# Kernel optimization log

Hardware: AMD Instinct MI355X
Metric: run time of the kernel (lower is better)

The kernel has to match this reference:

```python
import jax, jax.numpy as jnp
import numpy as np

B, L, D = 4, 8192, 512


def _normalize(v):
    # F.normalize: v / max(||v||, 1e-12)
    n = jnp.linalg.norm(v, axis=-1, keepdims=True)
    return v / jnp.maximum(n, 1e-12)


def setup_inputs() -> dict:
    key = jax.random.key(0)
    k1, k2, k3, k4 = jax.random.split(key, 4)
    return {
        "hidden_states": jax.random.normal(k1, (B, L, D), jnp.float32),
        "residual": jax.random.normal(k2, (B, L, D), jnp.float32),
        "q_weight": jax.random.normal(k3, (D, D), jnp.float32) * 0.02,
        "k_weight": jax.random.normal(k4, (D, D), jnp.float32) * 0.02,
        "det_state": jnp.zeros((B, D), jnp.float32),
    }


def reference(hidden_states, residual, q_weight, k_weight, det_state):
    Bs, Ls, Ds = hidden_states.shape
    # ---- CosineSimRouter.prob_boundary ----
    q = _normalize(hidden_states[:, :-1] @ q_weight.T)   # (B, L-1, D)
    k = _normalize(hidden_states[:, 1:] @ k_weight.T)    # (B, L-1, D)
    cos_sim = jnp.einsum('bld,bld->bl', q, k)            # (B, L-1)
    prob = jnp.concatenate(
        [jnp.ones((Bs, 1), jnp.float32), jnp.clip((1.0 - cos_sim) / 2.0, 0.0, 1.0)],
        axis=1)                                           # (B, L); prob[:,0]=1 (state=None path)
    token_mask = prob > 0.5                               # (B, L)

    # ---- Tokenizer: compact boundary positions (pad M -> L, static shape) ----
    counts = token_mask.sum(axis=1)                       # (B,)
    order = jnp.argsort(~token_mask, axis=1)              # stable: True-mask indices first, in order
    valid = jnp.arange(Ls)[None, :] < counts[:, None]     # (B, L)
    chunked = jnp.take_along_axis(hidden_states, order[..., None], axis=1)
    chunked = chunked * valid[..., None]                  # (B, L, D)
    chunk_probs = jnp.take_along_axis(prob, order, axis=1) * valid  # (B, L)

    # ---- DeTokenizer: EMA associative scan over compacted chunks ----
    decay = jnp.clip(1.0 - chunk_probs, 0.0, 1.0)
    # pad positions have chunk_probs=0 -> decay=1 -> state carried unchanged
    a = jnp.broadcast_to(decay[..., None], (Bs, Ls, Ds))
    b = (1.0 - decay)[..., None] * chunked
    b = b.at[:, 0].add(a[:, 0] * det_state)

    def comb(x, y):  # x earlier, y later: (a2*a1, a2*b1 + b2)
        ax, bx = x
        ay, by = y
        return ax * ay, ay * bx + by

    _, ema_out = jax.lax.associative_scan(comb, (a, b), axis=1)
    ema_out = ema_out * valid[..., None]                  # zero padded chunk slots

    # broadcast back to full sequence via cumulative chunk indexing
    chunk_idx = jnp.cumsum(token_mask.astype(jnp.int32), axis=1) - 1  # (B, L)
    ci = jnp.clip(chunk_idx, 0, Ls - 1)
    long_states = jnp.take_along_axis(ema_out, ci[..., None], axis=1)
    long_states = long_states * (chunk_idx >= 0)[..., None]

    # STE coefficient: forward == 1 (grad flows through max(1-p, p) in bwd)
    coef_raw = jnp.maximum(1.0 - prob, prob)
    coef = coef_raw + jax.lax.stop_gradient(1.0 - coef_raw)
    long_states = long_states * coef[..., None]

    output = residual + long_states                       # (B, L, D)
    return output
```

## Files before the change

### kernel.cpp

```cpp
#include <hip/hip_runtime.h>
#include <hip/hip_bf16.h>
#include <math.h>

#define B_  4
#define L_  8192
#define D_  512

#define BM   128
#define NCT  4
#define NRT  (L_ / BM)
#define KW   64
#define NSTAGE (D_ / KW)

#define CHUNK 64
#define NCHUNK (L_ / CHUNK)

#define MAXFIX 16380
#define FIX_TAU 1.0e-3f
#define FTILE 4

typedef short bf16x8 __attribute__((ext_vector_type(8)));
typedef float f32x4 __attribute__((ext_vector_type(4)));
typedef unsigned short u16;
typedef unsigned int u32;

__device__ __forceinline__ u32 pk2(float lo, float hi) {
    __hip_bfloat162 v = __float22bfloat162_rn(float2{lo, hi});
    union { __hip_bfloat162 b; u32 u; } cv; cv.b = v;
    return cv.u;
}

__global__ __launch_bounds__(256) void prep_w(
    const float* __restrict__ wq, const float* __restrict__ wk,
    u16* __restrict__ qh, u16* __restrict__ kh,
    float* __restrict__ wqt, float* __restrict__ wkt,
    int* __restrict__ fix_cnt)
{
    __shared__ float tile[64][65];
    const int bi = blockIdx.x;
    const int bj = blockIdx.y;
    const int t = threadIdx.x;
    if (bi == 0 && bj == 0 && t == 0) *fix_cnt = 0;
    const int c0 = bi * 64, k0 = bj * 64;
    const float* src = wq; float* dst = wqt; u16* dsth = qh;
#pragma unroll
    for (int m = 0; m < 2; ++m) {
        __syncthreads();
#pragma unroll
        for (int it = 0; it < 4; ++it) {
            int r = it * 16 + (t >> 4);
            int cc = (t & 15) * 4;
            float4 v = *(const float4*)(src + (size_t)(c0 + r) * D_ + k0 + cc);
            tile[r][cc] = v.x; tile[r][cc + 1] = v.y;
            tile[r][cc + 2] = v.z; tile[r][cc + 3] = v.w;
            uint2 hv; hv.x = pk2(v.x, v.y); hv.y = pk2(v.z, v.w);
            *(uint2*)(dsth + (size_t)(c0 + r) * D_ + k0 + cc) = hv;
        }
        __syncthreads();
#pragma unroll
        for (int it = 0; it < 4; ++it) {
            int cl = t & 63;
            int kq = it * 4 + (t >> 6);
            float4 v;
            v.x = tile[cl][kq * 4 + 0]; v.y = tile[cl][kq * 4 + 1];
            v.z = tile[cl][kq * 4 + 2]; v.w = tile[cl][kq * 4 + 3];
            size_t o = ((size_t)((k0 >> 2) + kq) * 512 + (c0 + cl)) * 4;
            *(float4*)(dst + o) = v;
        }
        src = wk; dst = wkt; dsth = kh;
    }
}

__global__ __launch_bounds__(256, 2) void qk_mfma(
    const float* __restrict__ h,
    const u16* __restrict__ wqh, const u16* __restrict__ wkh,
    float* __restrict__ part)
{
    const int bid = blockIdx.x;
    const int swz = (bid & 7) * 128 + (bid >> 3);
    const int ct = swz & 3, rt = (swz >> 2) & 63, b = swz >> 8;
    const int t = threadIdx.x, wid = t >> 6, lane = t & 63;
    const int l15 = lane & 15, l4 = lane >> 4;

    __shared__ __align__(16) u16 ah[129 * 64];
    __shared__ float red[4][BM][3];

    const int r0 = rt * BM;
    const float* hb = h + (size_t)b * L_ * D_;

    const int tr = t >> 4, q = t & 15;
    const float* gp = hb + (size_t)(r0 + tr) * D_ + q * 4;
    const int re = (r0 + BM > L_ - 1) ? (L_ - 1) : (r0 + BM);
    const float* gpe = hb + (size_t)re * D_ + q * 4;
    const int dbase = tr * 64 + (((q >> 1) ^ (tr & 7)) * 8) + ((q & 1) * 4);
    const int dE = 128 * 64 + ((t >> 1) * 8) + ((t & 1) * 4);

    const int colb = ct * 128 + wid * 32;
    const u16* bq0 = wqh + (size_t)(colb + l15) * D_ + l4 * 8;
    const u16* bq1 = bq0 + (size_t)16 * D_;
    const u16* bk0 = wkh + (size_t)(colb + l15) * D_ + l4 * 8;
    const u16* bk1 = bk0 + (size_t)16 * D_;

    int aoff[8];
#pragma unroll
    for (int rf = 0; rf < 8; ++rf) {
        int R = rf * 16 + l15;
        aoff[rf] = R * 64 + ((l4 ^ (R & 7)) * 8);
    }
    const int aoffE = 128 * 64 + l4 * 8;

    f32x4 accq[8][2], acck[8][2], ackl[2];
    const f32x4 zero = {0.f, 0.f, 0.f, 0.f};
#pragma unroll
    for (int rf = 0; rf < 8; ++rf) {
        accq[rf][0] = zero; accq[rf][1] = zero;
        acck[rf][0] = zero; acck[rf][1] = zero;
    }
    ackl[0] = zero; ackl[1] = zero;

    float4 A0, A1, A2, A3, A4, A5, A6, A7;
    float4 AE = {0.f, 0.f, 0.f, 0.f};

#define LOADA(S) do { const int _o = (S) * KW;                      \
    A0 = *(const float4*)(gp + _o);                                 \
    A1 = *(const float4*)(gp + _o + 8192);                          \
    A2 = *(const float4*)(gp + _o + 16384);                         \
    A3 = *(const float4*)(gp + _o + 24576);                         \
    A4 = *(const float4*)(gp + _o + 32768);                         \
    A5 = *(const float4*)(gp + _o + 40960);                         \
    A6 = *(const float4*)(gp + _o + 49152);                         \
    A7 = *(const float4*)(gp + _o + 57344);                         \
    if (t < 16) AE = *(const float4*)(gpe + _o); } while (0)

#define ST1(J, AV) { uint2 _h; _h.x = pk2(AV.x, AV.y); _h.y = pk2(AV.z, AV.w); \
    *(uint2*)(&ah[dbase + (J) * 1024]) = _h; }

    LOADA(0);
    for (int s = 0; s < NSTAGE; ++s) {
        __syncthreads();
        ST1(0, A0) ST1(1, A1) ST1(2, A2) ST1(3, A3)
        ST1(4, A4) ST1(5, A5) ST1(6, A6) ST1(7, A7)
        if (t < 16) { uint2 _h; _h.x = pk2(AE.x, AE.y); _h.y = pk2(AE.z, AE.w);
                      *(uint2*)(&ah[dE]) = _h; }

        const int so = s * KW;
        bf16x8 q00 = *(const bf16x8*)(bq0 + so);
        bf16x8 q01 = *(const bf16x8*)(bq0 + so + 32);
        bf16x8 q10 = *(const bf16x8*)(bq1 + so);
        bf16x8 q11 = *(const bf16x8*)(bq1 + so + 32);
        bf16x8 k00 = *(const bf16x8*)(bk0 + so);
        bf16x8 k01 = *(const bf16x8*)(bk0 + so + 32);
        bf16x8 k10 = *(const bf16x8*)(bk1 + so);
        bf16x8 k11 = *(const bf16x8*)(bk1 + so + 32);

        if (s + 1 < NSTAGE) LOADA(s + 1);
        __syncthreads();

#pragma unroll
        for (int kk = 0; kk < 2; ++kk) {
            bf16x8 fq0 = kk ? q01 : q00;
            bf16x8 fq1 = kk ? q11 : q10;
            bf16x8 fk0 = kk ? k01 : k00;
            bf16x8 fk1 = kk ? k11 : k10;
#pragma unroll
            for (int rf = 0; rf < 8; ++rf) {
                bf16x8 a = *(const bf16x8*)(&ah[aoff[rf] ^ (kk * 32)]);
                accq[rf][0] = __builtin_amdgcn_mfma_f32_16x16x32_bf16(a, fq0, accq[rf][0], 0, 0, 0);
                accq[rf][1] = __builtin_amdgcn_mfma_f32_16x16x32_bf16(a, fq1, accq[rf][1], 0, 0, 0);
                acck[rf][0] = __builtin_amdgcn_mfma_f32_16x16x32_bf16(a, fk0, acck[rf][0], 0, 0, 0);
                acck[rf][1] = __builtin_amdgcn_mfma_f32_16x16x32_bf16(a, fk1, acck[rf][1], 0, 0, 0);
            }
            bf16x8 al = *(const bf16x8*)(&ah[aoffE ^ (kk * 32)]);
            ackl[0] = __builtin_amdgcn_mfma_f32_16x16x32_bf16(al, fk0, ackl[0], 0, 0, 0);
            ackl[1] = __builtin_amdgcn_mfma_f32_16x16x32_bf16(al, fk1, ackl[1], 0, 0, 0);
        }
    }
#undef LOADA
#undef ST1

#pragma unroll
    for (int rf = 0; rf < 8; ++rf) {
#pragma unroll
        for (int reg = 0; reg < 4; ++reg) {
            float pq = 0.f, pk = 0.f, pd = 0.f;
#pragma unroll
            for (int cf = 0; cf < 2; ++cf) {
                float qv = accq[rf][cf][reg];
                float kv = acck[rf][cf][reg];
                pq += qv * qv;
                pk += kv * kv;
                float ksh;
                if (reg < 3) {
                    ksh = acck[rf][cf][reg + 1];
                } else {
                    float up = __shfl(acck[rf][cf][0], (lane + 16) & 63);
                    float nx0 = (rf < 7) ? acck[rf + 1][cf][0] : ackl[cf][0];
                    float nx = __shfl(nx0, l15);
                    ksh = (l4 == 3) ? nx : up;
                }
                pd += qv * ksh;
            }
#pragma unroll
            for (int off = 1; off < 16; off <<= 1) {
                pq += __shfl_xor(pq, off);
                pk += __shfl_xor(pk, off);
                pd += __shfl_xor(pd, off);
            }
            if (l15 == 0) {
                int row = rf * 16 + l4 * 4 + reg;
                red[wid][row][0] = pq;
                red[wid][row][1] = pk;
                red[wid][row][2] = pd;
            }
        }
    }
    __syncthreads();
    if (t < BM) {
        float pq = red[0][t][0] + red[1][t][0] + red[2][t][0] + red[3][t][0];
        float pk = red[0][t][1] + red[1][t][1] + red[2][t][1] + red[3][t][1];
        float pd = red[0][t][2] + red[1][t][2] + red[2][t][2] + red[3][t][2];
        size_t o = (((size_t)ct * B_ + b) * L_ + (r0 + t)) * 3;
        part[o + 0] = pq; part[o + 1] = pk; part[o + 2] = pd;
    }
}

__global__ __launch_bounds__(256) void cos_reduce(
    const float* __restrict__ part, float* __restrict__ p,
    int* __restrict__ fix_cnt, int* __restrict__ fix_list)
{
    int idx = blockIdx.x * 256 + threadIdx.x;
    if (idx >= B_ * L_) return;
    int b = idx / L_;
    int tp = idx % L_;
    if (tp == 0) { p[idx] = 1.0f; return; }
    int l = tp - 1;
    float nq = 0.f, nk = 0.f, dt = 0.f;
#pragma unroll
    for (int ct = 0; ct < NCT; ++ct) {
        size_t o = (((size_t)ct * B_ + b) * L_ + l) * 3;
        nq += part[o + 0];
        dt += part[o + 2];
        nk += part[o + 4];
    }
    float qn = sqrtf(nq); if (qn < 1e-12f) qn = 1e-12f;
    float kn = sqrtf(nk); if (kn < 1e-12f) kn = 1e-12f;
    float cs = dt / (qn * kn);
    float pr = 0.5f * (1.0f - cs);
    pr = fminf(fmaxf(pr, 0.0f), 1.0f);
    p[idx] = pr;
    if (fabsf(cs) < FIX_TAU) {
        int slot = atomicAdd(fix_cnt, 1);
        if (slot < MAXFIX) fix_list[slot] = idx;
    }
}

__global__ __launch_bounds__(256) void fixup_main(
    const float* __restrict__ h,
    const float* __restrict__ wqt, const float* __restrict__ wkt,
    const int* __restrict__ fix_cnt, const int* __restrict__ fix_list,
    float* __restrict__ p)
{
    __shared__ float hq[FTILE][D_];
    __shared__ float hk[FTILE][D_];
    __shared__ float red[FTILE][3][4];
    const int t = threadIdx.x, wid = t >> 6, lane = t & 63;
    int n = *fix_cnt; if (n > MAXFIX) n = MAXFIX;
    const int ntiles = (n + FTILE - 1) / FTILE;

    for (int tile = blockIdx.x; tile < ntiles; tile += gridDim.x) {
        __syncthreads();
#pragma unroll
        for (int r = 0; r < FTILE; ++r) {
            int s = tile * FTILE + r;
            int idx = fix_list[s < n ? s : 0];
            int bb = idx >> 13;
            int tp = idx & (L_ - 1);
            const float* hr = h + ((size_t)bb * L_ + (tp - 1)) * D_;
            ((float2*)hq[r])[t] = ((const float2*)hr)[t];
            ((float2*)hk[r])[t] = ((const float2*)(hr + D_))[t];
        }
        __syncthreads();

        float qa0[FTILE], qa1[FTILE], ka0[FTILE], ka1[FTILE];
#pragma unroll
        for (int r = 0; r < FTILE; ++r) { qa0[r] = qa1[r] = ka0[r] = ka1[r] = 0.f; }

        float4 wc0 = *(const float4*)(wqt + ((size_t)0 * 512 + t) * 4);
        float4 wc1 = *(const float4*)(wqt + ((size_t)0 * 512 + t + 256) * 4);
        float4 xc0 = *(const float4*)(wkt + ((size_t)0 * 512 + t) * 4);
        float4 xc1 = *(const float4*)(wkt + ((size_t)0 * 512 + t + 256) * 4);
#pragma unroll 4
        for (int kq = 0; kq < D_ / 4; ++kq) {
            const int kn = (kq + 1) & (D_ / 4 - 1);
            float4 wn0 = *(const float4*)(wqt + ((size_t)kn * 512 + t) * 4);
            float4 wn1 = *(const float4*)(wqt + ((size_t)kn * 512 + t + 256) * 4);
            float4 xn0 = *(const float4*)(wkt + ((size_t)kn * 512 + t) * 4);
            float4 xn1 = *(const float4*)(wkt + ((size_t)kn * 512 + t + 256) * 4);
#pragma unroll
            for (int r = 0; r < FTILE; ++r) {
                float4 hv = *(const float4*)(&hq[r][kq * 4]);
                float4 kv = *(const float4*)(&hk[r][kq * 4]);
                qa0[r] += hv.x * wc0.x + hv.y * wc0.y + hv.z * wc0.z + hv.w * wc0.w;
                qa1[r] += hv.x * wc1.x + hv.y * wc1.y + hv.z * wc1.z + hv.w * wc1.w;
                ka0[r] += kv.x * xc0.x + kv.y * xc0.y + kv.z * xc0.z + kv.w * xc0.w;
                ka1[r] += kv.x * xc1.x + kv.y * xc1.y + kv.z * xc1.z + kv.w * xc1.w;
            }
            wc0 = wn0; wc1 = wn1; xc0 = xn0; xc1 = xn1;
        }

#pragma unroll
        for (int r = 0; r < FTILE; ++r) {
            float pq = qa0[r] * qa0[r] + qa1[r] * qa1[r];
            float pk = ka0[r] * ka0[r] + ka1[r] * ka1[r];
            float pd = qa0[r] * ka0[r] + qa1[r] * ka1[r];
#pragma unroll
            for (int off = 1; off < 64; off <<= 1) {
                pq += __shfl_xor(pq, off);
                pk += __shfl_xor(pk, off);
                pd += __shfl_xor(pd, off);
            }
            if (lane == 0) { red[r][0][wid] = pq; red[r][1][wid] = pk; red[r][2][wid] = pd; }
        }
        __syncthreads();
        if (t < FTILE) {
            int s = tile * FTILE + t;
            if (s < n) {
                float nq = red[t][0][0] + red[t][0][1] + red[t][0][2] + red[t][0][3];
                float nk = red[t][1][0] + red[t][1][1] + red[t][1][2] + red[t][1][3];
                float dt = red[t][2][0] + red[t][2][1] + red[t][2][2] + red[t][2][3];
                float qn = sqrtf(nq); if (qn < 1e-12f) qn = 1e-12f;
                float kn = sqrtf(nk); if (kn < 1e-12f) kn = 1e-12f;
                float cs = dt / (qn * kn);
                float pr = 0.5f * (1.0f - cs);
                pr = fminf(fmaxf(pr, 0.0f), 1.0f);
                p[fix_list[s]] = pr;
            }
        }
    }
}

__global__ __launch_bounds__(256) void scan_a(
    const float* __restrict__ h, const float* __restrict__ p,
    float* __restrict__ Bc, float* __restrict__ Ac)
{
    const int t = threadIdx.x;
    const int c = blockIdx.x, b = blockIdx.y;
    const int l0 = c * CHUNK;
    const float* pb = p + (size_t)b * L_ + l0;
    const float2* hb = (const float2*)(h + ((size_t)b * L_ + l0) * D_) + t;

    float2 st = {0.f, 0.f};
    float ap = 1.f;
#pragma unroll 4
    for (int i = 0; i < CHUNK; ++i) {
        float pr = pb[i];
        float2 hv = hb[(size_t)i * 256];
        bool sel = pr > 0.5f;
        float a = sel ? 1.f - pr : 1.f;
        float g = sel ? pr : 0.f;
        st.x = a * st.x + g * hv.x;
        st.y = a * st.y + g * hv.y;
        ap *= a;
    }
    ((float2*)Bc)[((size_t)b * NCHUNK + c) * 256 + t] = st;
    if (t == 0) Ac[b * NCHUNK + c] = ap;
}

__global__ __launch_bounds__(256) void scan_b(
    const float* __restrict__ Ac, const float* __restrict__ Bc,
    const float* __restrict__ det, float* __restrict__ carry)
{
    const int t = threadIdx.x;
    const int b = blockIdx.x;
    const float* acb = Ac + b * NCHUNK;
    const float2* bcb = (const float2*)Bc + (size_t)b * NCHUNK * 256 + t;
    float2* cb = (float2*)carry + (size_t)b * NCHUNK * 256 + t;
    float2 st = ((const float2*)det)[(size_t)b * 256 + t];

    float a0 = acb[0], a1 = acb[1], a2 = acb[2], a3 = acb[3];
    float2 b0 = bcb[0], b1 = bcb[256], b2 = bcb[512], b3 = bcb[768];
    for (int g = 0; g < NCHUNK / 4; ++g) {
        const int nc = (g + 1 < NCHUNK / 4) ? (g + 1) * 4 : g * 4;
        float an0 = acb[nc], an1 = acb[nc + 1], an2 = acb[nc + 2], an3 = acb[nc + 3];
        float2 bn0 = bcb[(size_t)nc * 256],        bn1 = bcb[(size_t)(nc + 1) * 256];
        float2 bn2 = bcb[(size_t)(nc + 2) * 256],  bn3 = bcb[(size_t)(nc + 3) * 256];
        const size_t c0 = (size_t)g * 4 * 256;
        cb[c0]       = st; st.x = a0 * st.x + b0.x; st.y = a0 * st.y + b0.y;
        cb[c0 + 256] = st; st.x = a1 * st.x + b1.x; st.y = a1 * st.y + b1.y;
        cb[c0 + 512] = st; st.x = a2 * st.x + b2.x; st.y = a2 * st.y + b2.y;
        cb[c0 + 768] = st; st.x = a3 * st.x + b3.x; st.y = a3 * st.y + b3.y;
        a0 = an0; a1 = an1; a2 = an2; a3 = an3;
        b0 = bn0; b1 = bn1; b2 = bn2; b3 = bn3;
    }
}

__global__ __launch_bounds__(256) void scan_c(
    const float* __restrict__ h, const float* __restrict__ p,
    const float* __restrict__ res, const float* __restrict__ carry,
    float* __restrict__ out)
{
    const int t = threadIdx.x;
    const int c = blockIdx.x, b = blockIdx.y;
    const int l0 = c * CHUNK;
    const float* pb = p + (size_t)b * L_ + l0;
    const size_t base = ((size_t)b * L_ + l0) * 256 + t;
    const float2* hb = (const float2*)h + base;
    const float2* rb = (const float2*)res + base;
    float2* ob = (float2*)out + base;

    float2 st = ((const float2*)carry)[((size_t)b * NCHUNK + c) * 256 + t];
#pragma unroll 4
    for (int i = 0; i < CHUNK; ++i) {
        float pr = pb[i];
        float2 hv = hb[(size_t)i * 256];
        float2 rv = rb[(size_t)i * 256];
        bool sel = pr > 0.5f;
        float a = sel ? 1.f - pr : 1.f;
        float g = sel ? pr : 0.f;
        st.x = a * st.x + g * hv.x;
        st.y = a * st.y + g * hv.y;
        float2 ov; ov.x = rv.x + st.x; ov.y = rv.y + st.y;
        ob[(size_t)i * 256] = ov;
    }
}

extern "C" void kernel_launch(void* const* d_in, const int* in_sizes, int n_in,
                              void* d_out, int out_size, void* d_ws, size_t ws_size,
                              hipStream_t stream)
{
    const float* h   = (const float*)d_in[0];
    const float* res = (const float*)d_in[1];
    const float* wq  = (const float*)d_in[2];
    const float* wk  = (const float*)d_in[3];
    const float* det = (const float*)d_in[4];
    float* out = (float*)d_out;

    float* ws = (float*)d_ws;
    float* part  = ws;
    float* p     = part + (size_t)NCT * B_ * L_ * 3;
    float* Ac    = p + (size_t)B_ * L_;
    float* Bc    = Ac + (size_t)B_ * NCHUNK;
    float* carry = Bc + (size_t)B_ * NCHUNK * D_;
    int*  fix_cnt  = (int*)(carry + (size_t)B_ * NCHUNK * D_);
    int*  fix_list = fix_cnt + 4;
    u16* wqh = (u16*)(fix_list + MAXFIX);
    u16* wkh = wqh + (size_t)D_ * D_;
    float* wqt = (float*)(wkh + (size_t)D_ * D_);
    float* wkt = wqt + (size_t)D_ * D_;

    prep_w<<<dim3(8, 8), 256, 0, stream>>>(wq, wk, wqh, wkh, wqt, wkt, fix_cnt);
    qk_mfma<<<NCT * NRT * B_, 256, 0, stream>>>(h, wqh, wkh, part);
    cos_reduce<<<(B_ * L_ + 255) / 256, 256, 0, stream>>>(part, p, fix_cnt, fix_list);
    fixup_main<<<256, 256, 0, stream>>>(h, wqt, wkt, fix_cnt, fix_list, p);
    scan_a<<<dim3(NCHUNK, B_), 256, 0, stream>>>(h, p, Bc, Ac);
    scan_b<<<B_, 256, 0, stream>>>(Ac, Bc, det, carry);
    scan_c<<<dim3(NCHUNK, B_), 256, 0, stream>>>(h, p, res, carry, out);
}
```

Measured before the change: 201.7 us.

## Split fixup GEMV across column slices with partial reduce, relax qk_mfma barriers

The fp32 fixup kernel now processes 8 rows per tile and splits the 512 output columns into 4 work items per tile. Each wave half covers one half of the K range, so more blocks share the fixup work, and the 3 partial sums per slice go to a workspace. A new fixup_final kernel combines those slices into the probability. Separately, the qk_mfma main loop replaces __syncthreads with raw s_barrier plus sched_barrier and an explicit lgkmcnt wait, so global prefetch loads are not drained at each barrier. This adds an extra launch and workspace traffic, and the fixup work depends on how many near-zero cosine rows exist.

```diff
diff --git a/kernel.cpp b/kernel.cpp
--- a/kernel.cpp
+++ b/kernel.cpp
@@ -17,7 +17,7 @@
 
 #define MAXFIX 16380
 #define FIX_TAU 1.0e-3f
-#define FTILE 4
+#define FROWS 8
 
 typedef short bf16x8 __attribute__((ext_vector_type(8)));
 typedef float f32x4 __attribute__((ext_vector_type(4)));
@@ -137,7 +137,10 @@
 
     LOADA(0);
     for (int s = 0; s < NSTAGE; ++s) {
-        __syncthreads();
+        __builtin_amdgcn_sched_barrier(0);
+        __builtin_amdgcn_s_barrier();
+        __builtin_amdgcn_sched_barrier(0);
+
         ST1(0, A0) ST1(1, A1) ST1(2, A2) ST1(3, A3)
         ST1(4, A4) ST1(5, A5) ST1(6, A6) ST1(7, A7)
         if (t < 16) { uint2 _h; _h.x = pk2(AE.x, AE.y); _h.y = pk2(AE.z, AE.w);
@@ -154,7 +157,11 @@
         bf16x8 k11 = *(const bf16x8*)(bk1 + so + 32);
 
         if (s + 1 < NSTAGE) LOADA(s + 1);
-        __syncthreads();
+
+        asm volatile("s_waitcnt lgkmcnt(0)" ::: "memory");
+        __builtin_amdgcn_sched_barrier(0);
+        __builtin_amdgcn_s_barrier();
+        __builtin_amdgcn_sched_barrier(0);
 
 #pragma unroll
         for (int kk = 0; kk < 2; ++kk) {
@@ -258,20 +265,24 @@
     const float* __restrict__ h,
     const float* __restrict__ wqt, const float* __restrict__ wkt,
     const int* __restrict__ fix_cnt, const int* __restrict__ fix_list,
-    float* __restrict__ p)
-{
-    __shared__ float hq[FTILE][D_];
-    __shared__ float hk[FTILE][D_];
-    __shared__ float red[FTILE][3][4];
+    float* __restrict__ part_fix)
+{
+    __shared__ float hq[FROWS][D_];
+    __shared__ float hk[FROWS][D_];
+    __shared__ float red[FROWS][3][4];
     const int t = threadIdx.x, wid = t >> 6, lane = t & 63;
+    const int kh = lane >> 5;
     int n = *fix_cnt; if (n > MAXFIX) n = MAXFIX;
-    const int ntiles = (n + FTILE - 1) / FTILE;
-
-    for (int tile = blockIdx.x; tile < ntiles; tile += gridDim.x) {
+    const int ntiles = (n + FROWS - 1) / FROWS;
+    const int nitems = ntiles * 4;
+
+    for (int item = blockIdx.x; item < nitems; item += gridDim.x) {
+        const int tile = item >> 2;
+        const int cs = item & 3;
         __syncthreads();
 #pragma unroll
-        for (int r = 0; r < FTILE; ++r) {
-            int s = tile * FTILE + r;
+        for (int r = 0; r < FROWS; ++r) {
+            int s = tile * FROWS + r;
             int idx = fix_list[s < n ? s : 0];
             int bb = idx >> 13;
             int tp = idx & (L_ - 1);
@@ -281,61 +292,75 @@
         }
         __syncthreads();
 
-        float qa0[FTILE], qa1[FTILE], ka0[FTILE], ka1[FTILE];
-#pragma unroll
-        for (int r = 0; r < FTILE; ++r) { qa0[r] = qa1[r] = ka0[r] = ka1[r] = 0.f; }
-
-        float4 wc0 = *(const float4*)(wqt + ((size_t)0 * 512 + t) * 4);
-        float4 wc1 = *(const float4*)(wqt + ((size_t)0 * 512 + t + 256) * 4);
-        float4 xc0 = *(const float4*)(wkt + ((size_t)0 * 512 + t) * 4);
-        float4 xc1 = *(const float4*)(wkt + ((size_t)0 * 512 + t + 256) * 4);
+        const int c = cs * 128 + wid * 32 + (lane & 31);
+        float qa0, qa1, qa2, qa3, qa4, qa5, qa6, qa7;
+        float ka0, ka1, ka2, ka3, ka4, ka5, ka6, ka7;
+        qa0=qa1=qa2=qa3=qa4=qa5=qa6=qa7=0.f;
+        ka0=ka1=ka2=ka3=ka4=ka5=ka6=ka7=0.f;
+
+        const int k0 = kh * 64;
+        float4 wv = *(const float4*)(wqt + ((size_t)k0 * 512 + c) * 4);
+        float4 xv = *(const float4*)(wkt + ((size_t)k0 * 512 + c) * 4);
 #pragma unroll 4
-        for (int kq = 0; kq < D_ / 4; ++kq) {
-            const int kn = (kq + 1) & (D_ / 4 - 1);
-            float4 wn0 = *(const float4*)(wqt + ((size_t)kn * 512 + t) * 4);
-            float4 wn1 = *(const float4*)(wqt + ((size_t)kn * 512 + t + 256) * 4);
-            float4 xn0 = *(const float4*)(wkt + ((size_t)kn * 512 + t) * 4);
-            float4 xn1 = *(const float4*)(wkt + ((size_t)kn * 512 + t + 256) * 4);
-#pragma unroll
-            for (int r = 0; r < FTILE; ++r) {
-                float4 hv = *(const float4*)(&hq[r][kq * 4]);
-                float4 kv = *(const float4*)(&hk[r][kq * 4]);
-                qa0[r] += hv.x * wc0.x + hv.y * wc0.y + hv.z * wc0.z + hv.w * wc0.w;
-                qa1[r] += hv.x * wc1.x + hv.y * wc1.y + hv.z * wc1.z + hv.w * wc1.w;
-                ka0[r] += kv.x * xc0.x + kv.y * xc0.y + kv.z * xc0.z + kv.w * xc0.w;
-                ka1[r] += kv.x * xc1.x + kv.y * xc1.y + kv.z * xc1.z + kv.w * xc1.w;
+        for (int kq = k0; kq < k0 + 64; ++kq) {
+            const int kn = (kq + 1 < k0 + 64) ? kq + 1 : kq;
+            float4 wn = *(const float4*)(wqt + ((size_t)kn * 512 + c) * 4);
+            float4 xn = *(const float4*)(wkt + ((size_t)kn * 512 + c) * 4);
+#define FROW(R, QA, KA) { \
+            float4 hv = *(const float4*)(&hq[R][kq * 4]); \
+            float4 kv = *(const float4*)(&hk[R][kq * 4]); \
+            QA += hv.x*wv.x + hv.y*wv.y + hv.z*wv.z + hv.w*wv.w; \
+            KA += kv.x*xv.x + kv.y*xv.y + kv.z*xv.z + kv.w*xv.w; }
+            FROW(0, qa0, ka0) FROW(1, qa1, ka1) FROW(2, qa2, ka2) FROW(3, qa3, ka3)
+            FROW(4, qa4, ka4) FROW(5, qa5, ka5) FROW(6, qa6, ka6) FROW(7, qa7, ka7)
+#undef FROW
+            wv = wn; xv = xn;
+        }
+
+#define REDROW(R, QA, KA) { \
+        float qf = QA + __shfl_xor(QA, 32); \
+        float kf = KA + __shfl_xor(KA, 32); \
+        float pq = qf * qf, pk = kf * kf, pd = qf * kf; \
+        for (int off = 1; off < 32; off <<= 1) { \
+            pq += __shfl_xor(pq, off); \
+            pk += __shfl_xor(pk, off); \
+            pd += __shfl_xor(pd, off); \
+        } \
+        if (lane == 0) { red[R][0][wid] = pq; red[R][1][wid] = pk; red[R][2][wid] = pd; } }
+        REDROW(0, qa0, ka0) REDROW(1, qa1, ka1) REDROW(2, qa2, ka2) REDROW(3, qa3, ka3)
+        REDROW(4, qa4, ka4) REDROW(5, qa5, ka5) REDROW(6, qa6, ka6) REDROW(7, qa7, ka7)
+#undef REDROW
+        __syncthreads();
+        if (t < FROWS) {
+            int s = tile * FROWS + t;
+            if (s < n) {
+                float* pp = part_fix + ((size_t)s * 4 + cs) * 3;
+                pp[0] = red[t][0][0] + red[t][0][1] + red[t][0][2] + red[t][0][3];
+                pp[1] = red[t][1][0] + red[t][1][1] + red[t][1][2] + red[t][1][3];
+                pp[2] = red[t][2][0] + red[t][2][1] + red[t][2][2] + red[t][2][3];
             }
-            wc0 = wn0; wc1 = wn1; xc0 = xn0; xc1 = xn1;
-        }
-
-#pragma unroll
-        for (int r = 0; r < FTILE; ++r) {
-            float pq = qa0[r] * qa0[r] + qa1[r] * qa1[r];
-            float pk = ka0[r] * ka0[r] + ka1[r] * ka1[r];
-            float pd = qa0[r] * ka0[r] + qa1[r] * ka1[r];
-#pragma unroll
-            for (int off = 1; off < 64; off <<= 1) {
-                pq += __shfl_xor(pq, off);
-                pk += __shfl_xor(pk, off);
-                pd += __shfl_xor(pd, off);
-            }
-            if (lane == 0) { red[r][0][wid] = pq; red[r][1][wid] = pk; red[r][2][wid] = pd; }
-        }
-        __syncthreads();
-        if (t < FTILE) {
-            int s = tile * FTILE + t;
-            if (s < n) {
-                float nq = red[t][0][0] + red[t][0][1] + red[t][0][2] + red[t][0][3];
-                float nk = red[t][1][0] + red[t][1][1] + red[t][1][2] + red[t][1][3];
-                float dt = red[t][2][0] + red[t][2][1] + red[t][2][2] + red[t][2][3];
-                float qn = sqrtf(nq); if (qn < 1e-12f) qn = 1e-12f;
-                float kn = sqrtf(nk); if (kn < 1e-12f) kn = 1e-12f;
-                float cs = dt / (qn * kn);
-                float pr = 0.5f * (1.0f - cs);
-                pr = fminf(fmaxf(pr, 0.0f), 1.0f);
-                p[fix_list[s]] = pr;
-            }
-        }
+        }
+    }
+}
+
+__global__ __launch_bounds__(256) void fixup_final(
+    const int* __restrict__ fix_cnt, const int* __restrict__ fix_list,
+    const float* __restrict__ part_fix, float* __restrict__ p)
+{
+    int n = *fix_cnt; if (n > MAXFIX) n = MAXFIX;
+    for (int s = blockIdx.x * 256 + threadIdx.x; s < n; s += gridDim.x * 256) {
+        float nq = 0.f, nk = 0.f, dt = 0.f;
+#pragma unroll
+        for (int cs = 0; cs < 4; ++cs) {
+            const float* pp = part_fix + ((size_t)s * 4 + cs) * 3;
+            nq += pp[0]; nk += pp[1]; dt += pp[2];
+        }
+        float qn = sqrtf(nq); if (qn < 1e-12f) qn = 1e-12f;
+        float kn = sqrtf(nk); if (kn < 1e-12f) kn = 1e-12f;
+        float cs2 = dt / (qn * kn);
+        float pr = 0.5f * (1.0f - cs2);
+        pr = fminf(fmaxf(pr, 0.0f), 1.0f);
+        p[fix_list[s]] = pr;
     }
 }
 
@@ -447,11 +472,13 @@
     u16* wkh = wqh + (size_t)D_ * D_;
     float* wqt = (float*)(wkh + (size_t)D_ * D_);
     float* wkt = wqt + (size_t)D_ * D_;
+    float* part_fix = wkt + (size_t)D_ * D_;
 
     prep_w<<<dim3(8, 8), 256, 0, stream>>>(wq, wk, wqh, wkh, wqt, wkt, fix_cnt);
     qk_mfma<<<NCT * NRT * B_, 256, 0, stream>>>(h, wqh, wkh, part);
     cos_reduce<<<(B_ * L_ + 255) / 256, 256, 0, stream>>>(part, p, fix_cnt, fix_list);
-    fixup_main<<<256, 256, 0, stream>>>(h, wqt, wkt, fix_cnt, fix_list, p);
+    fixup_main<<<512, 256, 0, stream>>>(h, wqt, wkt, fix_cnt, fix_list, part_fix);
+    fixup_final<<<64, 256, 0, stream>>>(fix_cnt, fix_list, part_fix, p);
     scan_a<<<dim3(NCHUNK, B_), 256, 0, stream>>>(h, p, Bc, Ac);
     scan_b<<<B_, 256, 0, stream>>>(Ac, Bc, det, carry);
     scan_c<<<dim3(NCHUNK, B_), 256, 0, stream>>>(h, p, res, carry, out);
```

After: 180.8 us. 10.4% less time.
